# Kernel tuning notes

Hardware: AMD Instinct MI355X
Metric: run time of the kernel (lower is better)

Reference implementation:

```python
import jax, jax.numpy as jnp
import numpy as np

T, M, K, B, H, L, V = 64, 256, 6, 256, 256, 128, 780
E = T * M
PAD = E  # padding slot in hidden buffer = Lorentz origin

def _to_lorentz_np(s):
    t = np.sqrt(1.0 + (s * s).sum(-1, keepdims=True))
    return np.concatenate([t, s], -1).astype(np.float32)

def setup_inputs() -> dict:
    rng = np.random.default_rng(0)
    def make_nei():
        idx = np.full((T, M, K), PAD, np.int64)
        w = np.zeros((T, M, K), np.float32)
        for t in range(T):
            deg = rng.integers(0, K + 1, size=M)
            if t == 0:
                deg[:] = 0  # no messages exist yet
            mask = np.arange(K)[None, :] < deg[:, None]
            cand = rng.integers(0, max(1, t * M), size=(M, K))  # only already-computed slots
            idx[t] = np.where(mask, cand, PAD)
            w[t] = mask.astype(np.float32)
            w[t, deg == 0, 0] = 1.0  # zero-neighbor case -> use origin padding (as in torch code)
        return idx.astype(np.int32), w
    nei_h_idx, nei_h_w = make_nei()
    nei_o_idx, nei_o_w = make_nei()
    return dict(
        wid=jnp.asarray(rng.integers(0, V, size=(T, M)), jnp.int32),
        nei_h_idx=jnp.asarray(nei_h_idx), nei_h_w=jnp.asarray(nei_h_w),
        nei_o_idx=jnp.asarray(nei_o_idx), nei_o_w=jnp.asarray(nei_o_w),
        batch_idx=jnp.asarray(rng.integers(0, B, size=(T, M)), jnp.int32),
        direction=jnp.asarray(rng.integers(0, 2, size=(T, M)), jnp.int32),
        pred_target=jnp.asarray(rng.integers(0, V, size=(T, M)), jnp.int32),
        root_wid=jnp.asarray(rng.integers(0, V, size=(B,)), jnp.int32),
        root_o_idx=jnp.asarray(rng.integers(0, E, size=(B, K)), jnp.int32),
        root_o_w=jnp.ones((B, K), jnp.float32),
        x_tree_vecs=jnp.asarray(_to_lorentz_np(rng.standard_normal((B, L - 1)) * 0.5)),
        embedding=jnp.asarray(_to_lorentz_np(rng.standard_normal((V, H - 1)) * 0.5)),
        W0=jnp.asarray(rng.standard_normal((H, H)) * 0.02, dtype=jnp.float32),
        b0=jnp.zeros((H,), jnp.float32),
        s0=jnp.asarray(np.log(10.0), jnp.float32),
        W1=jnp.asarray(rng.standard_normal((H, 2 * H - 1)) * 0.02, dtype=jnp.float32),
        b1=jnp.zeros((H,), jnp.float32),
        s1=jnp.asarray(np.log(10.0), jnp.float32),
        wcls=jnp.asarray(_to_lorentz_np(rng.standard_normal((V, H + L - 2)) * 0.5)),
        wbias=jnp.zeros((V,), jnp.float32),
        ucls=jnp.asarray(_to_lorentz_np(rng.standard_normal((2, 2 * H + L - 3)) * 0.5)),
        ubias=jnp.zeros((2,), jnp.float32),
    )

def _llinear(x, W, b, scale):
    # LorentzLinear: affine map, then rescale space part so output stays on the hyperboloid
    x = x @ W.T + b
    xs = x[..., 1:]
    time = jax.nn.sigmoid(x[..., :1]) * jnp.exp(scale) + 1.1
    sq = (time * time - 1.0) / jnp.clip((xs * xs).sum(-1, keepdims=True), 1e-8)
    return jnp.concatenate([time, xs * jnp.sqrt(sq)], -1)

def _mid_point(x, w):
    # Lorentz centroid: weighted mean renormalized to the manifold. x: [...,K,d], w: [...,K]
    ave = jnp.einsum('...k,...kd->...d', w, x) / jnp.clip(w.sum(-1, keepdims=True), 1e-8)
    inner = (ave[..., 1:] ** 2).sum(-1, keepdims=True) - ave[..., :1] ** 2  # <ave,ave>_L
    return ave / jnp.sqrt(jnp.clip(-inner, 1e-8))

def _concat(x, y):
    # hyperbolic concat: keep space parts, recompute time (dim = d1+d2-1)
    time = jnp.sqrt(jnp.clip(x[..., :1] ** 2 + y[..., :1] ** 2 - 1.0, 1e-8))
    return jnp.concatenate([time, x[..., 1:], y[..., 1:]], -1)

def _centroid(x, cls_pts, bias):
    # LorentzCentroidDistance logits: 2 + 2*<x, c>_L + bias
    inner = x[..., 1:] @ cls_pts[:, 1:].T - x[..., :1] * cls_pts[None, :, 0]
    return 2.0 + 2.0 * inner + bias

def _ce(scores, tgt):
    lp = jax.nn.log_softmax(scores, -1)
    return -jnp.take_along_axis(lp, tgt[:, None], axis=-1)[:, 0]

def _forward_core(wid, nei_h_idx, nei_h_w, nei_o_idx, nei_o_w, batch_idx, direction,
                  pred_target, root_wid, root_o_idx, root_o_w, x_tree_vecs, embedding,
                  W0, b0, s0, W1, b1, s1, wcls, wbias, ucls, ubias):
    hbuf0 = jnp.zeros((E + 1, H), jnp.float32).at[:, 0].set(1.0)  # all origin; slot E is padding

    def step(carry, xs_t):
        hbuf, t = carry
        wid_t, idx_t, w_t = xs_t
        cur_x = embedding[wid_t]                      # [M,H]
        h_nei = hbuf[idx_t]                           # [M,K,H] gather of prior messages
        h1 = _llinear(h_nei, W0, b0, s0)              # A0
        h1m = _mid_point(h1, w_t)                     # [M,H]
        new_h = _llinear(_concat(cur_x, h1m), W1, b1, s1)  # A1
        hbuf = jax.lax.dynamic_update_slice(hbuf, new_h, (t * M, 0))
        return (hbuf, t + jnp.int32(1)), new_h

    (hbuf, _), new_h = jax.lax.scan(step, (hbuf0, jnp.int32(0)), (wid, nei_h_idx, nei_h_w))
    new_h = new_h.reshape(E, H)
    cur_x = embedding[wid.reshape(E)]
    cur_o = _mid_point(hbuf[nei_o_idx.reshape(E, K)], nei_o_w.reshape(E, K))
    ctx = x_tree_vecs[batch_idx.reshape(E)]

    # word prediction: roots (origin hidden) + forward-direction messages
    origin = jnp.zeros((B, H), jnp.float32).at[:, 0].set(1.0)
    root_scores = _centroid(_concat(origin, x_tree_vecs), wcls, wbias)   # [B,V]
    msg_scores = _centroid(_concat(new_h, ctx), wcls, wbias)             # [E,V]
    pmask = direction.reshape(E).astype(jnp.float32)
    pt = pred_target.reshape(E)
    pred_loss = (_ce(root_scores, root_wid).sum() + (pmask * _ce(msg_scores, pt)).sum()) / B
    pred_hit = ((jnp.argmax(root_scores, -1) == root_wid).astype(jnp.float32).sum()
                + (pmask * (jnp.argmax(msg_scores, -1) == pt).astype(jnp.float32)).sum())
    pred_acc = pred_hit / (B + pmask.sum())

    # stop prediction: every message + final per-tree root entry (target 0)
    stop_h = _concat(_concat(cur_x, cur_o), ctx)                         # [E, 2H+L-2]
    root_o = _mid_point(hbuf[root_o_idx], root_o_w)
    stop_root = _concat(_concat(embedding[root_wid], root_o), x_tree_vecs)
    stop_scores = _centroid(jnp.concatenate([stop_h, stop_root], 0), ucls, ubias)
    stop_tgt = jnp.concatenate([direction.reshape(E), jnp.zeros((B,), jnp.int32)], 0)
    stop_loss = _ce(stop_scores, stop_tgt).sum() / B
    stop_acc = (jnp.argmax(stop_scores, -1) == stop_tgt).astype(jnp.float32).mean()
    return pred_loss, stop_loss, pred_acc, stop_acc

def reference(wid, nei_h_idx, nei_h_w, nei_o_idx, nei_o_w, batch_idx, direction,
              pred_target, root_wid, root_o_idx, root_o_w, x_tree_vecs, embedding,
              W0, b0, s0, W1, b1, s1, wcls, wbias, ucls, ubias):
    return _forward_core(wid, nei_h_idx, nei_h_w, nei_o_idx, nei_o_w, batch_idx, direction,
                         pred_target, root_wid, root_o_idx, root_o_w, x_tree_vecs, embedding,
                         W0, b0, s0, W1, b1, s1, wcls, wbias, ucls, ubias)
```

## Files before the change

### kernel.cpp

```cpp
#include <hip/hip_runtime.h>
#include <math.h>

#define T_ 64
#define M_ 256
#define K_ 6
#define B_ 256
#define H_ 256
#define L_ 128
#define V_ 780
#define E_ (T_*M_)
#define ZD 383
#define UD 638
#define KP 384
#define VP 832
#define TAG_PAD 0x7fffffffu

typedef unsigned short ushort_t;
typedef __attribute__((ext_vector_type(8))) _Float16 half8v;
typedef __attribute__((ext_vector_type(4))) _Float16 half4v;
typedef __attribute__((ext_vector_type(2))) _Float16 half2v;
typedef __attribute__((ext_vector_type(4))) float f32x4v;
typedef unsigned long long u64;


__device__ __forceinline__ float blk_sum(float v, float* red) {
    int j = threadIdx.x;
    #pragma unroll
    for (int o = 32; o > 0; o >>= 1) v += __shfl_down(v, o, 64);
    __syncthreads();
    if ((j & 63) == 0) red[j >> 6] = v;
    __syncthreads();
    return red[0] + red[1] + red[2] + red[3];
}

__device__ __forceinline__ float wave_sum(float v) {
    #pragma unroll
    for (int o = 32; o > 0; o >>= 1) v += __shfl_xor(v, o, 64);
    return v;
}

__device__ __forceinline__ _Float16 f2h(float x) { return (_Float16)x; }

__device__ __forceinline__ u64 llc_load8(const u64* p) {
    return __hip_atomic_load(p, __ATOMIC_RELAXED, __HIP_MEMORY_SCOPE_AGENT);
}
__device__ __forceinline__ void llc_store8(u64* p, u64 v) {
    __hip_atomic_store(p, v, __ATOMIC_RELAXED, __HIP_MEMORY_SCOPE_AGENT);
}


#define PREP_R0 ((E_ + 1) * H_)
#define PREP_RT ((E_ + 1) * 128)
#define PREP_R1 65536
#define PREP_R2 65536
#define PREP_R3 (VP * KP)
#define PREP_R4 65536
#define PREP_TOTAL (PREP_R0 + PREP_RT + PREP_R1 + PREP_R2 + PREP_R3 + PREP_R4)

__global__ __launch_bounds__(256) void prep_k(const float* __restrict__ W0,
                                              const float* __restrict__ W1,
                                              const float* __restrict__ wcls,
                                              float* __restrict__ hbuf,
                                              u64* __restrict__ hbuf2,
                                              _Float16* __restrict__ W0P,
                                              _Float16* __restrict__ W1HP,
                                              _Float16* __restrict__ Wh,
                                              float* __restrict__ W1T) {
    int idx = blockIdx.x * 256 + threadIdx.x;
    if (idx < PREP_R0) {
        hbuf[idx] = (idx >= E_ * H_ && (idx & (H_ - 1)) == 0) ? 1.f : 0.f;
        return;
    }
    idx -= PREP_R0;
    if (idx < PREP_RT) {
        int row = idx >> 7, cp = idx & 127;
        u64 val = 0ull;
        if (row == E_) {
            unsigned int lo = (cp == 0) ? 0x3C00u : 0u;
            val = ((u64)TAG_PAD << 32) | lo;
        }
        hbuf2[idx] = val;
        return;
    }
    idx -= PREP_RT;
    if (idx < PREP_R1) {
        int e = idx & 7, l = (idx >> 3) & 63, ks = (idx >> 9) & 7, nt = idx >> 12;
        int jj = nt * 16 + (l & 15);
        int ii = ks * 32 + (l >> 4) * 8 + e;
        W0P[idx] = f2h(W0[(size_t)jj * H_ + ii]);
        return;
    }
    idx -= PREP_R1;
    if (idx < PREP_R2) {
        int e = idx & 7, l = (idx >> 3) & 63, ks = (idx >> 9) & 7, nt = idx >> 12;
        int jj = nt * 16 + (l & 15);
        int ii = ks * 32 + (l >> 4) * 8 + e;
        float v = (ii == 0) ? W1[(size_t)jj * (2 * H_ - 1)]
                            : W1[(size_t)jj * (2 * H_ - 1) + 255 + ii];
        W1HP[idx] = f2h(v);
        return;
    }
    idx -= PREP_R2;
    if (idx < PREP_R3) {
        int v = idx / KP, k = idx - v * KP;
        float val = (v < V_ && k < ZD) ? wcls[(size_t)v * ZD + k] : 0.f;
        Wh[idx] = f2h(val);
        return;
    }
    idx -= PREP_R3;
    if (idx < PREP_R4) {
        int i = idx >> 8, j = idx & 255;
        W1T[idx] = (i >= 1) ? W1[(size_t)j * (2 * H_ - 1) + i] : 0.f;
    }
}


__global__ __launch_bounds__(256) void basew_k(const float* __restrict__ emb,
                                               const float* __restrict__ W1T,
                                               const float* __restrict__ b1,
                                               float* __restrict__ basew) {
    int v = blockIdx.x, j = threadIdx.x;
    __shared__ float cxs[256];
    cxs[j] = emb[(size_t)v * H_ + j];
    __syncthreads();
    float acc = b1[j];
    #pragma unroll 8
    for (int i = 1; i < 256; i++) acc = fmaf(cxs[i], W1T[i * 256 + j], acc);
    basew[(size_t)v * H_ + j] = acc;
}


__global__ __launch_bounds__(256, 1) void scan_flow(float* __restrict__ hbuf,
        u64* __restrict__ hbuf2,
        const _Float16* __restrict__ W0P, const float* __restrict__ b0, const float* __restrict__ s0p,
        const _Float16* __restrict__ W1HP, const float* __restrict__ s1p,
        const float* __restrict__ emb, const int* __restrict__ wid,
        const int* __restrict__ nhi, const float* __restrict__ nhw,
        const float* __restrict__ basew) {
    int tid = threadIdx.x;
    int w = tid >> 6, l = tid & 63;
    int quad = l >> 4, col = l & 15;
    int m = blockIdx.x;
    int j0 = 4 * l;
    int cp = tid & 127;
    int rsel = tid >> 7;

    __shared__ __align__(16) _Float16 hn16[16][264];
    __shared__ __align__(16) _Float16 zzs[4][264];
    __shared__ __align__(16) float Ys[6][256];
    __shared__ __align__(16) float y2s[256];

    half8v w0f[4][8], w1f[4][8];
    #pragma unroll
    for (int q = 0; q < 4; q++) {
        int nt = 4 * w + q;
        #pragma unroll
        for (int ks = 0; ks < 8; ks++) {
            w0f[q][ks] = *(const half8v*)(W0P + ((size_t)(nt * 8 + ks) * 64 + l) * 8);
            w1f[q][ks] = *(const half8v*)(W1HP + ((size_t)(nt * 8 + ks) * 64 + l) * 8);
        }
    }

    float es0 = expf(s0p[0]);
    float es1 = expf(s1p[0]);
    float4 bj4 = *(const float4*)(b0 + j0);

    unsigned int tagx[3];
    const u64* pp[3];
    u64 pvv[3];
    #pragma unroll
    for (int p = 0; p < 3; p++) {
        int row = 2 * p + rsel;
        int id = nhi[(size_t)m * K_ + row];
        tagx[p] = (id < E_) ? (unsigned int)(id >> 8) + 1u : TAG_PAD;
        pp[p] = hbuf2 + ((size_t)id << 7) + cp;
        pvv[p] = llc_load8(pp[p]);
    }

    for (int t = 0; t < T_; t++) {
        int e = t * M_ + m;
        const float* wp = nhw + e * K_;

        float wk[K_];
        #pragma unroll
        for (int k = 0; k < K_; k++) wk[k] = wp[k];
        int wde = wid[e];
        float4 bw4 = *(const float4*)(basew + (size_t)wde * H_ + j0);
        float cx0 = emb[(size_t)wde * H_];

        for (;;) {
            bool ok = ((unsigned int)(pvv[0] >> 32) == tagx[0])
                   && ((unsigned int)(pvv[1] >> 32) == tagx[1])
                   && ((unsigned int)(pvv[2] >> 32) == tagx[2]);
            if (ok) break;
            __builtin_amdgcn_s_sleep(1);
            #pragma unroll
            for (int p = 0; p < 3; p++)
                if ((unsigned int)(pvv[p] >> 32) != tagx[p]) pvv[p] = llc_load8(pp[p]);
        }
        #pragma unroll
        for (int p = 0; p < 3; p++)
            *(unsigned int*)&hn16[2 * p + rsel][cp * 2] = (unsigned int)pvv[p];
        __syncthreads();

        if (t + 1 < T_) {
            #pragma unroll
            for (int p = 0; p < 3; p++) {
                int row = 2 * p + rsel;
                int id = nhi[(size_t)(e + M_) * K_ + row];
                tagx[p] = (id < E_) ? (unsigned int)(id >> 8) + 1u : TAG_PAD;
                pp[p] = hbuf2 + ((size_t)id << 7) + cp;
                pvv[p] = llc_load8(pp[p]);
            }
        }

        f32x4v acc[4];
        #pragma unroll
        for (int q = 0; q < 4; q++) acc[q] = (f32x4v){0.f, 0.f, 0.f, 0.f};
        #pragma unroll
        for (int ks = 0; ks < 8; ks++) {
            half8v afr = *(const half8v*)&hn16[col][ks * 32 + quad * 8];
            #pragma unroll
            for (int q = 0; q < 4; q++)
                acc[q] = __builtin_amdgcn_mfma_f32_16x16x32_f16(afr, w0f[q][ks], acc[q], 0, 0, 0);
        }
        #pragma unroll
        for (int q = 0; q < 4; q++) {
            int nt = 4 * w + q;
            #pragma unroll
            for (int rr = 0; rr < 4; rr++) {
                int row = quad * 4 + rr;
                if (row < 6) Ys[row][nt * 16 + col] = acc[q][rr];
            }
        }
        __syncthreads();

        float y[K_][4];
        #pragma unroll
        for (int k = 0; k < K_; k++) {
            float4 yv = *(const float4*)&Ys[k][j0];
            y[k][0] = yv.x + bj4.x; y[k][1] = yv.y + bj4.y;
            y[k][2] = yv.z + bj4.z; y[k][3] = yv.w + bj4.w;
        }
        float c[K_];
        #pragma unroll
        for (int k = 0; k < K_; k++) {
            float cc = y[k][0] * y[k][0] + y[k][1] * y[k][1]
                     + y[k][2] * y[k][2] + y[k][3] * y[k][3];
            if (l == 0) cc -= y[k][0] * y[k][0];
            c[k] = cc;
        }
        #pragma unroll
        for (int o = 32; o > 0; o >>= 1) {
            #pragma unroll
            for (int k = 0; k < K_; k++) c[k] += __shfl_xor(c[k], o, 64);
        }
        float y0b[K_];
        #pragma unroll
        for (int k = 0; k < K_; k++) y0b[k] = __shfl(y[k][0], 0, 64);

        float ave[4] = {0.f, 0.f, 0.f, 0.f};
        float wsum = 0.f;
        #pragma unroll
        for (int k = 0; k < K_; k++) {
            float tm = es0 / (1.f + expf(-y0b[k])) + 1.1f;
            float sc = sqrtf((tm * tm - 1.f) / fmaxf(c[k], 1e-8f));
            #pragma unroll
            for (int c2 = 0; c2 < 4; c2++) {
                float h1v = (l == 0 && c2 == 0) ? tm : y[k][c2] * sc;
                ave[c2] += wk[k] * h1v;
            }
            wsum += wk[k];
        }
        float inv = 1.f / fmaxf(wsum, 1e-8f);
        float innl = 0.f;
        #pragma unroll
        for (int c2 = 0; c2 < 4; c2++) { ave[c2] *= inv; innl += ave[c2] * ave[c2]; }
        if (l == 0) innl -= 2.f * ave[0] * ave[0];
        float inner = wave_sum(innl);
        float rsc = 1.f / sqrtf(fmaxf(-inner, 1e-8f));

        #pragma unroll
        for (int c2 = 0; c2 < 4; c2++) {
            int j = j0 + c2;
            float h1m = ave[c2] * rsc;
            if (j == 0) {
                zzs[w][0] = f2h(sqrtf(fmaxf(cx0 * cx0 + h1m * h1m - 1.f, 1e-8f)));
            } else {
                zzs[w][j] = f2h(h1m);
            }
        }

        f32x4v a2[4];
        #pragma unroll
        for (int q = 0; q < 4; q++) a2[q] = (f32x4v){0.f, 0.f, 0.f, 0.f};
        #pragma unroll
        for (int ks = 0; ks < 8; ks++) {
            half8v zfr = *(const half8v*)&zzs[w][ks * 32 + quad * 8];
            #pragma unroll
            for (int q = 0; q < 4; q++)
                a2[q] = __builtin_amdgcn_mfma_f32_16x16x32_f16(zfr, w1f[q][ks], a2[q], 0, 0, 0);
        }
        if (quad == 0) {
            #pragma unroll
            for (int q = 0; q < 4; q++) y2s[(4 * w + q) * 16 + col] = a2[q][0];
        }
        __syncthreads();

        if (w == 0) {
            float4 y2v = *(const float4*)&y2s[j0];
            float y2[4] = {y2v.x + bw4.x, y2v.y + bw4.y, y2v.z + bw4.z, y2v.w + bw4.w};
            float c2s = y2[0] * y2[0] + y2[1] * y2[1] + y2[2] * y2[2] + y2[3] * y2[3];
            if (l == 0) c2s -= y2[0] * y2[0];
            float ssq2 = wave_sum(c2s);
            float y20 = __shfl(y2[0], 0, 64);
            float tm2 = es1 / (1.f + expf(-y20)) + 1.1f;
            float sc2 = sqrtf((tm2 * tm2 - 1.f) / fmaxf(ssq2, 1e-8f));
            float hv0 = (l == 0) ? tm2 : y2[0] * sc2;
            float hv1 = y2[1] * sc2, hv2 = y2[2] * sc2, hv3 = y2[3] * sc2;

            unsigned int tag = (unsigned int)t + 1u;
            union { half2v h; unsigned int u; } c01, c23;
            c01.h.x = f2h(hv0); c01.h.y = f2h(hv1);
            c23.h.x = f2h(hv2); c23.h.y = f2h(hv3);
            u64* pb = hbuf2 + ((size_t)e << 7) + 2 * l;
            llc_store8(pb,     ((u64)tag << 32) | c01.u);
            llc_store8(pb + 1, ((u64)tag << 32) | c23.u);

            float4 out4 = {hv0, hv1, hv2, hv3};
            *(float4*)(hbuf + (size_t)e * H_ + j0) = out4;
        }
    }
}


__global__ __launch_bounds__(256) void zbuild2(const float* __restrict__ hbuf,
                                               const float* __restrict__ xtv,
                                               const int* __restrict__ bidx,
                                               _Float16* __restrict__ Zh) {
    int e = blockIdx.x, j = threadIdx.x;
    int bi = bidx[e];
    _Float16* zr = Zh + (size_t)e * KP;
    if (j == 0) {
        float nh0 = hbuf[(size_t)e * H_];
        float c0  = xtv[(size_t)bi * L_];
        float z0  = sqrtf(fmaxf(nh0 * nh0 + c0 * c0 - 1.f, 1e-8f));
        zr[0] = f2h(-z0);
    } else {
        zr[j] = f2h(hbuf[(size_t)e * H_ + j]);
    }
    if (j < 128) {
        int c = 256 + j;
        float v = (c <= 382) ? xtv[(size_t)bi * L_ + (c - 255)] : 0.f;
        zr[c] = f2h(v);
    }
}


__global__ __launch_bounds__(256) void gemm_ce(const _Float16* __restrict__ Zh,
                                               const _Float16* __restrict__ Wh,
                                               const float* __restrict__ wbias,
                                               const int* __restrict__ pt,
                                               const int* __restrict__ dir,
                                               float* __restrict__ part) {
    __shared__ __align__(16) _Float16 As[64][392];
    __shared__ __align__(16) _Float16 Bsf[64][392];
    __shared__ __align__(16) float SCs[64][68];
    __shared__ float rmax[64], rsum[64], rval[64];
    __shared__ int   rargi[64];

    int tid = threadIdx.x;
    int w = tid >> 6, l = tid & 63;
    int r16 = l & 15, quad = l >> 4;
    int q8 = quad * 8;
    int m0 = blockIdx.x * 64;

    #pragma unroll
    for (int i = 0; i < 12; i++) {
        int u = tid + i * 256;
        int row = u / 48, c8 = (u % 48) * 8;
        *(uint4*)&As[row][c8] = *(const uint4*)(Zh + (size_t)(m0 + row) * KP + c8);
    }
    if (tid < 64) {
        rmax[tid] = -1e30f; rsum[tid] = 0.f; rargi[tid] = 0; rval[tid] = 0.f;
    }
    __syncthreads();

    for (int nt = 0; nt < 13; nt++) {
        int n0 = nt * 64;
        #pragma unroll
        for (int i = 0; i < 12; i++) {
            int u = tid + i * 256;
            int row = u / 48, c8 = (u % 48) * 8;
            *(uint4*)&Bsf[row][c8] = *(const uint4*)(Wh + (size_t)(n0 + row) * KP + c8);
        }
        __syncthreads();

        f32x4v acc[4];
        #pragma unroll
        for (int mt = 0; mt < 4; mt++) acc[mt] = (f32x4v){0.f, 0.f, 0.f, 0.f};
        #pragma unroll
        for (int ks = 0; ks < 12; ks++) {
            half8v bfr = *(const half8v*)&Bsf[w * 16 + r16][ks * 32 + q8];
            #pragma unroll
            for (int mt = 0; mt < 4; mt++) {
                half8v afr = *(const half8v*)&As[mt * 16 + r16][ks * 32 + q8];
                acc[mt] = __builtin_amdgcn_mfma_f32_16x16x32_f16(afr, bfr, acc[mt], 0, 0, 0);
            }
        }
        int ncol = n0 + w * 16 + r16;
        float bias = (ncol < V_) ? wbias[ncol] : 0.f;
        #pragma unroll
        for (int mt = 0; mt < 4; mt++) {
            #pragma unroll
            for (int rr = 0; rr < 4; rr++)
                SCs[mt * 16 + quad * 4 + rr][w * 16 + r16] = 2.f + 2.f * acc[mt][rr] + bias;
        }
        __syncthreads();

        {
            int row = tid >> 2, prt = tid & 3;
            int tg = pt[m0 + row];
            float vals[16];
            float lm = -1e30f; int li = 0;
            #pragma unroll
            for (int c = 0; c < 16; c++) {
                int nc = n0 + prt * 16 + c;
                float x = (nc < V_) ? SCs[row][prt * 16 + c] : -1e30f;
                vals[c] = x;
                if (x > lm) { lm = x; li = nc; }
                if (nc == tg) rval[row] = x;
            }
            #pragma unroll
            for (int o = 1; o < 4; o <<= 1) {
                float om = __shfl_xor(lm, o, 64);
                int   oi = __shfl_xor(li, o, 64);
                if (om > lm || (om == lm && oi < li)) { lm = om; li = oi; }
            }
            float ls = 0.f;
            #pragma unroll
            for (int c = 0; c < 16; c++) {
                int nc = n0 + prt * 16 + c;
                if (nc < V_) ls += expf(vals[c] - lm);
            }
            #pragma unroll
            for (int o = 1; o < 4; o <<= 1) ls += __shfl_xor(ls, o, 64);
            if (prt == 0) {
                float om = rmax[row], os = rsum[row];
                float nm = fmaxf(om, lm);
                rsum[row] = os * expf(om - nm) + ls * expf(lm - nm);
                if (lm > om) rargi[row] = li;
                rmax[row] = nm;
            }
        }
        __syncthreads();
    }

    if (tid < 64) {
        int e = m0 + tid;
        int tg = pt[e];
        float pm = (float)dir[e];
        float lse = rmax[tid] + logf(rsum[tid]);
        float lloss = pm * (lse - rval[tid]);
        float lhit  = pm * ((rargi[tid] == tg) ? 1.f : 0.f);
        float lpm   = pm;
        lloss = wave_sum(lloss);
        lhit  = wave_sum(lhit);
        lpm   = wave_sum(lpm);
        if (tid == 0) {
            float* pr = part + (size_t)blockIdx.x * 8;
            pr[0] = lloss; pr[1] = lhit; pr[2] = lpm;
            pr[3] = 0.f; pr[4] = 0.f;
        }
    }
}


__global__ __launch_bounds__(256) void stoproot_k(const float* __restrict__ hbuf,
        const float* __restrict__ emb, const float* __restrict__ xtv,
        const int* __restrict__ wid, const int* __restrict__ noi, const float* __restrict__ now_w,
        const int* __restrict__ bidx, const int* __restrict__ dir,
        const int* __restrict__ rwid, const int* __restrict__ roi, const float* __restrict__ row_w,
        const float* __restrict__ wcls, const float* __restrict__ wbias,
        const float* __restrict__ ucls, const float* __restrict__ ubias,
        float* __restrict__ part) {
    __shared__ float red[256];
    __shared__ int   redi[256];
    __shared__ float shs[4];
    __shared__ float ctxs[L_];
    __shared__ float sc[V_];
    __shared__ float red2[4][2];

    if (blockIdx.x < 256) {
        int w = threadIdx.x >> 6, l = threadIdx.x & 63;
        int wg = blockIdx.x * 4 + w;

        float ua0[4], ub0[4], ua1[4], ub1[4], uc0[2], uc1[2];
        #pragma unroll
        for (int s = 0; s < 4; s++) {
            int j = s * 64 + l;
            ua0[s] = ucls[j];        ub0[s] = ucls[255 + j];
            ua1[s] = ucls[UD + j];   ub1[s] = ucls[UD + 255 + j];
        }
        #pragma unroll
        for (int s = 0; s < 2; s++) {
            int j = s * 64 + l;
            uc0[s] = ucls[510 + j];  uc1[s] = ucls[UD + 510 + j];
        }
        float u00 = ucls[0], u10 = ucls[UD];
        float ubs0 = ubias[0], ubs1 = ubias[1];

        float lloss = 0.f, lhit = 0.f;
        for (int i = 0; i < 16; i++) {
            int e = wg * 16 + i;
            const int*   ip = noi + e * K_;
            const float* wp = now_w + e * K_;
            float ave[4] = {0.f, 0.f, 0.f, 0.f};
            float wsum = 0.f;
            #pragma unroll
            for (int k = 0; k < K_; k++) {
                int id = ip[k]; float wt = wp[k];
                wsum += wt;
                const float* hr = hbuf + (size_t)id * H_;
                #pragma unroll
                for (int s = 0; s < 4; s++) ave[s] += wt * hr[s * 64 + l];
            }
            float inv = 1.f / fmaxf(wsum, 1e-8f);
            float innl = 0.f;
            #pragma unroll
            for (int s = 0; s < 4; s++) { ave[s] *= inv; innl += ave[s] * ave[s]; }
            if (l == 0) innl -= 2.f * ave[0] * ave[0];
            float inner = wave_sum(innl);
            float cs = 1.f / sqrtf(fmaxf(-inner, 1e-8f));

            int we = wid[e], bi = bidx[e];
            const float* er = emb + (size_t)we * H_;
            const float* cr = xtv + (size_t)bi * L_;

            float p0 = 0.f, p1 = 0.f;
            #pragma unroll
            for (int s = 0; s < 4; s++) {
                float cx = er[s * 64 + l];
                float co = ave[s] * cs;
                if (s == 0 && l == 0) {
                    float ctx0 = cr[0];
                    float t1sq = fmaxf(cx * cx + co * co - 1.f, 1e-8f);
                    float sh0 = sqrtf(fmaxf(t1sq + ctx0 * ctx0 - 1.f, 1e-8f));
                    p0 += -sh0 * u00; p1 += -sh0 * u10;
                } else {
                    p0 += cx * ua0[s] + co * ub0[s];
                    p1 += cx * ua1[s] + co * ub1[s];
                }
                if (s < 2) {
                    int j = s * 64 + l;
                    if (j >= 1) {
                        float ctx = cr[j];
                        p0 += ctx * uc0[s]; p1 += ctx * uc1[s];
                    }
                }
            }
            p0 = wave_sum(p0); p1 = wave_sum(p1);
            if (l == 0) {
                float sc0 = 2.f + 2.f * p0 + ubs0;
                float sc1 = 2.f + 2.f * p1 + ubs1;
                int tgt = dir[e];
                float mm = fmaxf(sc0, sc1);
                float lse = mm + logf(expf(sc0 - mm) + expf(sc1 - mm));
                lloss += lse - ((tgt == 0) ? sc0 : sc1);
                int am = (sc1 > sc0) ? 1 : 0;
                lhit += (am == tgt) ? 1.f : 0.f;
            }
        }
        if (l == 0) { red2[w][0] = lloss; red2[w][1] = lhit; }
        __syncthreads();
        if (threadIdx.x == 0) {
            float* pr = part + (size_t)(256 + blockIdx.x) * 8;
            pr[0] = 0.f; pr[1] = 0.f; pr[2] = 0.f;
            pr[3] = red2[0][0] + red2[1][0] + red2[2][0] + red2[3][0];
            pr[4] = red2[0][1] + red2[1][1] + red2[2][1] + red2[3][1];
        }
    } else {
        int b = blockIdx.x - 256, j = threadIdx.x;
        float* pr = part + (size_t)(512 + b) * 8;

        const int*   ip = roi + b * K_;
        const float* wp = row_w + b * K_;
        float ave = 0.f, wsum = 0.f;
        #pragma unroll
        for (int k = 0; k < K_; k++) {
            int id = ip[k]; float w = wp[k];
            ave += w * hbuf[(size_t)id * H_ + j];
            wsum += w;
        }
        ave /= fmaxf(wsum, 1e-8f);
        float inner = blk_sum((j == 0) ? -ave * ave : ave * ave, red);
        float ro = ave / sqrtf(fmaxf(-inner, 1e-8f));

        int   rw = rwid[b];
        float er = emb[(size_t)rw * H_ + j];
        float ctxj = (j < L_) ? xtv[(size_t)b * L_ + j] : 0.f;
        if (j == 0) { shs[0] = er; shs[1] = ro; shs[2] = ctxj; }
        if (j < L_) ctxs[j] = ctxj;
        __syncthreads();
        float t1sq = fmaxf(shs[0] * shs[0] + shs[1] * shs[1] - 1.f, 1e-8f);
        float sh0  = sqrtf(fmaxf(t1sq + shs[2] * shs[2] - 1.f, 1e-8f));

        float p0, p1;
        if (j >= 1) {
            p0 = er * ucls[j] + ro * ucls[255 + j];
            p1 = er * ucls[UD + j] + ro * ucls[UD + 255 + j];
            if (j < L_) { p0 += ctxj * ucls[510 + j]; p1 += ctxj * ucls[UD + 510 + j]; }
        } else {
            p0 = -sh0 * ucls[0];
            p1 = -sh0 * ucls[UD];
        }
        float s0 = 2.f + 2.f * blk_sum(p0, red) + ubias[0];
        float s1 = 2.f + 2.f * blk_sum(p1, red) + ubias[1];
        if (j == 0) {
            float mm = fmaxf(s0, s1);
            float lse = mm + logf(expf(s0 - mm) + expf(s1 - mm));
            int am = (s1 > s0) ? 1 : 0;
            pr[3] = lse - s0;
            pr[4] = (am == 0) ? 1.f : 0.f;
        }

        float c0 = shs[2];
        float z0 = sqrtf(fmaxf(c0 * c0, 1e-8f));
        __syncthreads();
        for (int v = j; v < V_; v += 256) {
            const float* wv = wcls + (size_t)v * ZD;
            float d = -z0 * wv[0];
            for (int i = 1; i < L_; i++) d += ctxs[i] * wv[255 + i];
            sc[v] = 2.f + 2.f * d + wbias[v];
        }
        __syncthreads();
        float mx = -1e30f; int mi = 0;
        for (int v = j; v < V_; v += 256) { float x = sc[v]; if (x > mx) { mx = x; mi = v; } }
        red[j] = mx; redi[j] = mi;
        __syncthreads();
        for (int o = 128; o > 0; o >>= 1) {
            if (j < o) {
                float xo = red[j + o]; int io = redi[j + o];
                if (xo > red[j] || (xo == red[j] && io < redi[j])) { red[j] = xo; redi[j] = io; }
            }
            __syncthreads();
        }
        float gm = red[0]; int ga = redi[0];
        __syncthreads();
        float se = 0.f;
        for (int v = j; v < V_; v += 256) se += expf(sc[v] - gm);
        red[j] = se;
        __syncthreads();
        for (int o = 128; o > 0; o >>= 1) { if (j < o) red[j] += red[j + o]; __syncthreads(); }
        if (j == 0) {
            float lse = gm + logf(red[0]);
            pr[0] = lse - sc[rw];
            pr[1] = (ga == rw) ? 1.f : 0.f;
            pr[2] = 0.f;
        }
    }
}


__global__ __launch_bounds__(256) void finalize2(const float* __restrict__ part,
                                                 float* __restrict__ out) {
    int j = threadIdx.x;
    __shared__ float red[256][5];
    #pragma unroll
    for (int c = 0; c < 5; c++)
        red[j][c] = part[(size_t)j * 8 + c] + part[(size_t)(j + 256) * 8 + c]
                  + part[(size_t)(j + 512) * 8 + c];
    __syncthreads();
    for (int o = 128; o > 0; o >>= 1) {
        if (j < o) {
            #pragma unroll
            for (int c = 0; c < 5; c++) red[j][c] += red[j + o][c];
        }
        __syncthreads();
    }
    if (j == 0) {
        out[0] = red[0][0] / (float)B_;
        out[1] = red[0][3] / (float)B_;
        out[2] = red[0][1] / ((float)B_ + red[0][2]);
        out[3] = red[0][4] / (float)(E_ + B_);
    }
}


extern "C" void kernel_launch(void* const* d_in, const int* in_sizes, int n_in,
                              void* d_out, int out_size, void* d_ws, size_t ws_size,
                              hipStream_t stream) {
    const int*   wid   = (const int*)d_in[0];
    const int*   nhi   = (const int*)d_in[1];
    const float* nhw   = (const float*)d_in[2];
    const int*   noi   = (const int*)d_in[3];
    const float* now_w = (const float*)d_in[4];
    const int*   bidx  = (const int*)d_in[5];
    const int*   dir   = (const int*)d_in[6];
    const int*   pt    = (const int*)d_in[7];
    const int*   rwid  = (const int*)d_in[8];
    const int*   roi   = (const int*)d_in[9];
    const float* row_w = (const float*)d_in[10];
    const float* xtv   = (const float*)d_in[11];
    const float* emb   = (const float*)d_in[12];
    const float* W0    = (const float*)d_in[13];
    const float* b0    = (const float*)d_in[14];
    const float* s0    = (const float*)d_in[15];
    const float* W1    = (const float*)d_in[16];
    const float* b1    = (const float*)d_in[17];
    const float* s1    = (const float*)d_in[18];
    const float* wcls  = (const float*)d_in[19];
    const float* wbias = (const float*)d_in[20];
    const float* ucls  = (const float*)d_in[21];
    const float* ubias = (const float*)d_in[22];

    float* ws    = (float*)d_ws;
    float* hbuf  = ws;
    u64*   hbuf2 = (u64*)(hbuf + (size_t)(E_ + 1) * H_);
    float* part  = (float*)(hbuf2 + (size_t)(E_ + 1) * 128);
    float* basew = part + 768 * 8;
    float* W1T   = basew + (size_t)V_ * H_;
    _Float16* W0P  = (_Float16*)(W1T + 65536);
    _Float16* W1HP = W0P + 65536;
    _Float16* Zh   = W1HP + 65536;
    _Float16* Wh   = Zh + (size_t)E_ * KP;
    float* out  = (float*)d_out;

    prep_k<<<(PREP_TOTAL + 255) / 256, 256, 0, stream>>>(W0, W1, wcls, hbuf, hbuf2,
                                                         W0P, W1HP, Wh, W1T);
    basew_k<<<V_, 256, 0, stream>>>(emb, W1T, b1, basew);

    scan_flow<<<M_, 256, 0, stream>>>(hbuf, hbuf2, W0P, b0, s0, W1HP, s1,
                                      emb, wid, nhi, nhw, basew);

    zbuild2<<<E_, 256, 0, stream>>>(hbuf, xtv, bidx, Zh);
    gemm_ce<<<256, 256, 0, stream>>>(Zh, Wh, wbias, pt, dir, part);
    stoproot_k<<<512, 256, 0, stream>>>(hbuf, emb, xtv, wid, noi, now_w, bidx, dir,
                                        rwid, roi, row_w, wcls, wbias, ucls, ubias, part);
    finalize2<<<1, 256, 0, stream>>>(part, out);
}
```

Before: 589.5 us.

## Fuse Z-build and prediction GEMM+CE into scan kernel tail with tag-polled handoff

Drops the zbuild2 and gemm_ce launches. After its scan loop, each scan_flow block polls tagged fp16 hidden rows for its 64-row tile, builds the fp16 Z tile in shared memory and runs the MFMA GEMM with online softmax cross-entropy. It also stops zero-initialising the full fp32 hidden buffer, writing only the padding row, and adds a per-row tagged h0 buffer. The aim is to cut launch overhead and the Zh round trip through global memory and to overlap the tail with the scan, at the cost of much more LDS per block and spin-waiting on other blocks' results.

```diff
diff --git a/kernel.cpp b/kernel.cpp
--- a/kernel.cpp
+++ b/kernel.cpp
@@ -49,26 +49,28 @@
 }
 
 
-#define PREP_R0 ((E_ + 1) * H_)
+#define PREP_R0 H_
 #define PREP_RT ((E_ + 1) * 128)
+#define PREP_RH3 E_
 #define PREP_R1 65536
 #define PREP_R2 65536
 #define PREP_R3 (VP * KP)
 #define PREP_R4 65536
-#define PREP_TOTAL (PREP_R0 + PREP_RT + PREP_R1 + PREP_R2 + PREP_R3 + PREP_R4)
+#define PREP_TOTAL (PREP_R0 + PREP_RT + PREP_RH3 + PREP_R1 + PREP_R2 + PREP_R3 + PREP_R4)
 
 __global__ __launch_bounds__(256) void prep_k(const float* __restrict__ W0,
                                               const float* __restrict__ W1,
                                               const float* __restrict__ wcls,
                                               float* __restrict__ hbuf,
                                               u64* __restrict__ hbuf2,
+                                              u64* __restrict__ hbuf3,
                                               _Float16* __restrict__ W0P,
                                               _Float16* __restrict__ W1HP,
                                               _Float16* __restrict__ Wh,
                                               float* __restrict__ W1T) {
     int idx = blockIdx.x * 256 + threadIdx.x;
     if (idx < PREP_R0) {
-        hbuf[idx] = (idx >= E_ * H_ && (idx & (H_ - 1)) == 0) ? 1.f : 0.f;
+        hbuf[(size_t)E_ * H_ + idx] = (idx == 0) ? 1.f : 0.f;
         return;
     }
     idx -= PREP_R0;
@@ -83,6 +85,11 @@
         return;
     }
     idx -= PREP_RT;
+    if (idx < PREP_RH3) {
+        hbuf3[idx] = 0ull;
+        return;
+    }
+    idx -= PREP_RH3;
     if (idx < PREP_R1) {
         int e = idx & 7, l = (idx >> 3) & 63, ks = (idx >> 9) & 7, nt = idx >> 12;
         int jj = nt * 16 + (l & 15);
@@ -131,12 +138,16 @@
 
 
 __global__ __launch_bounds__(256, 1) void scan_flow(float* __restrict__ hbuf,
-        u64* __restrict__ hbuf2,
+        u64* __restrict__ hbuf2, u64* __restrict__ hbuf3,
         const _Float16* __restrict__ W0P, const float* __restrict__ b0, const float* __restrict__ s0p,
         const _Float16* __restrict__ W1HP, const float* __restrict__ s1p,
         const float* __restrict__ emb, const int* __restrict__ wid,
         const int* __restrict__ nhi, const float* __restrict__ nhw,
-        const float* __restrict__ basew) {
+        const float* __restrict__ basew,
+        const _Float16* __restrict__ Wh, const float* __restrict__ wbias,
+        const int* __restrict__ pt, const int* __restrict__ dir,
+        const int* __restrict__ bidx, const float* __restrict__ xtv,
+        float* __restrict__ part) {
     int tid = threadIdx.x;
     int w = tid >> 6, l = tid & 63;
     int quad = l >> 4, col = l & 15;
@@ -149,6 +160,11 @@
     __shared__ __align__(16) _Float16 zzs[4][264];
     __shared__ __align__(16) float Ys[6][256];
     __shared__ __align__(16) float y2s[256];
+    __shared__ __align__(16) _Float16 As[64][392];
+    __shared__ __align__(16) _Float16 Bsf[64][392];
+    __shared__ __align__(16) float SCs[64][68];
+    __shared__ float rmax[64], rsum[64], rval[64];
+    __shared__ int   rargi[64];
 
     half8v w0f[4][8], w1f[4][8];
     #pragma unroll
@@ -327,150 +343,166 @@
             llc_store8(pb,     ((u64)tag << 32) | c01.u);
             llc_store8(pb + 1, ((u64)tag << 32) | c23.u);
 
+            if (l == 0) {
+                union { float f; unsigned int u; } h0b; h0b.f = tm2;
+                llc_store8(hbuf3 + e, ((u64)tag << 32) | h0b.u);
+            }
+
             float4 out4 = {hv0, hv1, hv2, hv3};
             *(float4*)(hbuf + (size_t)e * H_ + j0) = out4;
         }
     }
-}
-
-
-__global__ __launch_bounds__(256) void zbuild2(const float* __restrict__ hbuf,
-                                               const float* __restrict__ xtv,
-                                               const int* __restrict__ bidx,
-                                               _Float16* __restrict__ Zh) {
-    int e = blockIdx.x, j = threadIdx.x;
-    int bi = bidx[e];
-    _Float16* zr = Zh + (size_t)e * KP;
-    if (j == 0) {
-        float nh0 = hbuf[(size_t)e * H_];
-        float c0  = xtv[(size_t)bi * L_];
-        float z0  = sqrtf(fmaxf(nh0 * nh0 + c0 * c0 - 1.f, 1e-8f));
-        zr[0] = f2h(-z0);
-    } else {
-        zr[j] = f2h(hbuf[(size_t)e * H_ + j]);
-    }
-    if (j < 128) {
-        int c = 256 + j;
-        float v = (c <= 382) ? xtv[(size_t)bi * L_ + (c - 255)] : 0.f;
-        zr[c] = f2h(v);
-    }
-}
-
-
-__global__ __launch_bounds__(256) void gemm_ce(const _Float16* __restrict__ Zh,
-                                               const _Float16* __restrict__ Wh,
-                                               const float* __restrict__ wbias,
-                                               const int* __restrict__ pt,
-                                               const int* __restrict__ dir,
-                                               float* __restrict__ part) {
-    __shared__ __align__(16) _Float16 As[64][392];
-    __shared__ __align__(16) _Float16 Bsf[64][392];
-    __shared__ __align__(16) float SCs[64][68];
-    __shared__ float rmax[64], rsum[64], rval[64];
-    __shared__ int   rargi[64];
-
-    int tid = threadIdx.x;
-    int w = tid >> 6, l = tid & 63;
-    int r16 = l & 15, quad = l >> 4;
-    int q8 = quad * 8;
-    int m0 = blockIdx.x * 64;
-
-    #pragma unroll
-    for (int i = 0; i < 12; i++) {
-        int u = tid + i * 256;
-        int row = u / 48, c8 = (u % 48) * 8;
-        *(uint4*)&As[row][c8] = *(const uint4*)(Zh + (size_t)(m0 + row) * KP + c8);
-    }
-    if (tid < 64) {
-        rmax[tid] = -1e30f; rsum[tid] = 0.f; rargi[tid] = 0; rval[tid] = 0.f;
-    }
-    __syncthreads();
-
-    for (int nt = 0; nt < 13; nt++) {
-        int n0 = nt * 64;
-        #pragma unroll
-        for (int i = 0; i < 12; i++) {
-            int u = tid + i * 256;
-            int row = u / 48, c8 = (u % 48) * 8;
-            *(uint4*)&Bsf[row][c8] = *(const uint4*)(Wh + (size_t)(n0 + row) * KP + c8);
-        }
-        __syncthreads();
-
-        f32x4v acc[4];
-        #pragma unroll
-        for (int mt = 0; mt < 4; mt++) acc[mt] = (f32x4v){0.f, 0.f, 0.f, 0.f};
-        #pragma unroll
-        for (int ks = 0; ks < 12; ks++) {
-            half8v bfr = *(const half8v*)&Bsf[w * 16 + r16][ks * 32 + q8];
+
+    {
+        int m0 = m * 64;
+
+        u64 gpv[32];
+        #pragma unroll
+        for (int i = 0; i < 32; i++) {
+            int p = tid + i * 256;
+            int row = p >> 7, cpp = p & 127;
+            gpv[i] = llc_load8(hbuf2 + ((size_t)(m0 + row) << 7) + cpp);
+        }
+        for (;;) {
+            bool ok = true;
+            #pragma unroll
+            for (int i = 0; i < 32; i++) {
+                int row = (tid + i * 256) >> 7;
+                unsigned int tg = (unsigned int)((m0 + row) >> 8) + 1u;
+                if ((unsigned int)(gpv[i] >> 32) != tg) ok = false;
+            }
+            if (ok) break;
+            __builtin_amdgcn_s_sleep(1);
+            #pragma unroll
+            for (int i = 0; i < 32; i++) {
+                int p = tid + i * 256;
+                int row = p >> 7, cpp = p & 127;
+                unsigned int tg = (unsigned int)((m0 + row) >> 8) + 1u;
+                if ((unsigned int)(gpv[i] >> 32) != tg)
+                    gpv[i] = llc_load8(hbuf2 + ((size_t)(m0 + row) << 7) + cpp);
+            }
+        }
+        #pragma unroll
+        for (int i = 0; i < 32; i++) {
+            int p = tid + i * 256;
+            int row = p >> 7, cpp = p & 127;
+            *(unsigned int*)&As[row][2 * cpp] = (unsigned int)gpv[i];
+        }
+        #pragma unroll
+        for (int i = 0; i < 16; i++) {
+            int p = tid + i * 256;
+            int row = p >> 6, k2 = (p & 63) * 2;
+            int bi = bidx[m0 + row];
+            int ca = 256 + k2;
+            half2v hv;
+            hv.x = (ca <= 382) ? f2h(xtv[(size_t)bi * L_ + (ca - 255)]) : (_Float16)0.f;
+            hv.y = (ca + 1 <= 382) ? f2h(xtv[(size_t)bi * L_ + (ca - 254)]) : (_Float16)0.f;
+            *(half2v*)&As[row][ca] = hv;
+        }
+        if (tid < 64) {
+            int e2 = m0 + tid;
+            unsigned int tg = (unsigned int)(e2 >> 8) + 1u;
+            u64 hv3 = llc_load8(hbuf3 + e2);
+            while ((unsigned int)(hv3 >> 32) != tg) {
+                __builtin_amdgcn_s_sleep(1);
+                hv3 = llc_load8(hbuf3 + e2);
+            }
+            union { unsigned int u; float f; } h0c; h0c.u = (unsigned int)hv3;
+            int bi = bidx[e2];
+            float c0 = xtv[(size_t)bi * L_];
+            float z0 = sqrtf(fmaxf(h0c.f * h0c.f + c0 * c0 - 1.f, 1e-8f));
+            As[tid][0] = f2h(-z0);
+            rmax[tid] = -1e30f; rsum[tid] = 0.f; rargi[tid] = 0; rval[tid] = 0.f;
+        }
+        __syncthreads();
+
+        int q8 = quad * 8;
+        for (int nt = 0; nt < 13; nt++) {
+            int n0 = nt * 64;
+            #pragma unroll
+            for (int i = 0; i < 12; i++) {
+                int uu = tid + i * 256;
+                int row = uu / 48, c8 = (uu % 48) * 8;
+                *(uint4*)&Bsf[row][c8] = *(const uint4*)(Wh + (size_t)(n0 + row) * KP + c8);
+            }
+            __syncthreads();
+
+            f32x4v gacc[4];
+            #pragma unroll
+            for (int mt = 0; mt < 4; mt++) gacc[mt] = (f32x4v){0.f, 0.f, 0.f, 0.f};
+            #pragma unroll
+            for (int ks = 0; ks < 12; ks++) {
+                half8v bfr = *(const half8v*)&Bsf[w * 16 + col][ks * 32 + q8];
+                #pragma unroll
+                for (int mt = 0; mt < 4; mt++) {
+                    half8v afr = *(const half8v*)&As[mt * 16 + col][ks * 32 + q8];
+                    gacc[mt] = __builtin_amdgcn_mfma_f32_16x16x32_f16(afr, bfr, gacc[mt], 0, 0, 0);
+                }
+            }
+            int ncol = n0 + w * 16 + col;
+            float bias = (ncol < V_) ? wbias[ncol] : 0.f;
             #pragma unroll
             for (int mt = 0; mt < 4; mt++) {
-                half8v afr = *(const half8v*)&As[mt * 16 + r16][ks * 32 + q8];
-                acc[mt] = __builtin_amdgcn_mfma_f32_16x16x32_f16(afr, bfr, acc[mt], 0, 0, 0);
-            }
-        }
-        int ncol = n0 + w * 16 + r16;
-        float bias = (ncol < V_) ? wbias[ncol] : 0.f;
-        #pragma unroll
-        for (int mt = 0; mt < 4; mt++) {
-            #pragma unroll
-            for (int rr = 0; rr < 4; rr++)
-                SCs[mt * 16 + quad * 4 + rr][w * 16 + r16] = 2.f + 2.f * acc[mt][rr] + bias;
-        }
-        __syncthreads();
-
-        {
-            int row = tid >> 2, prt = tid & 3;
-            int tg = pt[m0 + row];
-            float vals[16];
-            float lm = -1e30f; int li = 0;
-            #pragma unroll
-            for (int c = 0; c < 16; c++) {
-                int nc = n0 + prt * 16 + c;
-                float x = (nc < V_) ? SCs[row][prt * 16 + c] : -1e30f;
-                vals[c] = x;
-                if (x > lm) { lm = x; li = nc; }
-                if (nc == tg) rval[row] = x;
-            }
-            #pragma unroll
-            for (int o = 1; o < 4; o <<= 1) {
-                float om = __shfl_xor(lm, o, 64);
-                int   oi = __shfl_xor(li, o, 64);
-                if (om > lm || (om == lm && oi < li)) { lm = om; li = oi; }
-            }
-            float ls = 0.f;
-            #pragma unroll
-            for (int c = 0; c < 16; c++) {
-                int nc = n0 + prt * 16 + c;
-                if (nc < V_) ls += expf(vals[c] - lm);
-            }
-            #pragma unroll
-            for (int o = 1; o < 4; o <<= 1) ls += __shfl_xor(ls, o, 64);
-            if (prt == 0) {
-                float om = rmax[row], os = rsum[row];
-                float nm = fmaxf(om, lm);
-                rsum[row] = os * expf(om - nm) + ls * expf(lm - nm);
-                if (lm > om) rargi[row] = li;
-                rmax[row] = nm;
-            }
-        }
-        __syncthreads();
-    }
-
-    if (tid < 64) {
-        int e = m0 + tid;
-        int tg = pt[e];
-        float pm = (float)dir[e];
-        float lse = rmax[tid] + logf(rsum[tid]);
-        float lloss = pm * (lse - rval[tid]);
-        float lhit  = pm * ((rargi[tid] == tg) ? 1.f : 0.f);
-        float lpm   = pm;
-        lloss = wave_sum(lloss);
-        lhit  = wave_sum(lhit);
-        lpm   = wave_sum(lpm);
-        if (tid == 0) {
-            float* pr = part + (size_t)blockIdx.x * 8;
-            pr[0] = lloss; pr[1] = lhit; pr[2] = lpm;
-            pr[3] = 0.f; pr[4] = 0.f;
+                #pragma unroll
+                for (int rr = 0; rr < 4; rr++)
+                    SCs[mt * 16 + quad * 4 + rr][w * 16 + col] = 2.f + 2.f * gacc[mt][rr] + bias;
+            }
+            __syncthreads();
+
+            {
+                int row = tid >> 2, prt = tid & 3;
+                int tg = pt[m0 + row];
+                float vals[16];
+                float lm = -1e30f; int li = 0;
+                #pragma unroll
+                for (int cc = 0; cc < 16; cc++) {
+                    int nc = n0 + prt * 16 + cc;
+                    float x = (nc < V_) ? SCs[row][prt * 16 + cc] : -1e30f;
+                    vals[cc] = x;
+                    if (x > lm) { lm = x; li = nc; }
+                    if (nc == tg) rval[row] = x;
+                }
+                #pragma unroll
+                for (int o = 1; o < 4; o <<= 1) {
+                    float om = __shfl_xor(lm, o, 64);
+                    int   oi = __shfl_xor(li, o, 64);
+                    if (om > lm || (om == lm && oi < li)) { lm = om; li = oi; }
+                }
+                float ls = 0.f;
+                #pragma unroll
+                for (int cc = 0; cc < 16; cc++) {
+                    int nc = n0 + prt * 16 + cc;
+                    if (nc < V_) ls += expf(vals[cc] - lm);
+                }
+                #pragma unroll
+                for (int o = 1; o < 4; o <<= 1) ls += __shfl_xor(ls, o, 64);
+                if (prt == 0) {
+                    float om = rmax[row], os = rsum[row];
+                    float nm = fmaxf(om, lm);
+                    rsum[row] = os * expf(om - nm) + ls * expf(lm - nm);
+                    if (lm > om) rargi[row] = li;
+                    rmax[row] = nm;
+                }
+            }
+            __syncthreads();
+        }
+
+        if (tid < 64) {
+            int e2 = m0 + tid;
+            int tg = pt[e2];
+            float pm = (float)dir[e2];
+            float lse = rmax[tid] + logf(rsum[tid]);
+            float lloss = pm * (lse - rval[tid]);
+            float lhit  = pm * ((rargi[tid] == tg) ? 1.f : 0.f);
+            float lpm   = pm;
+            lloss = wave_sum(lloss);
+            lhit  = wave_sum(lhit);
+            lpm   = wave_sum(lpm);
+            if (tid == 0) {
+                float* pr = part + (size_t)m * 8;
+                pr[0] = lloss; pr[1] = lhit; pr[2] = lpm;
+                pr[3] = 0.f; pr[4] = 0.f;
+            }
         }
     }
 }
@@ -717,24 +749,23 @@
     float* ws    = (float*)d_ws;
     float* hbuf  = ws;
     u64*   hbuf2 = (u64*)(hbuf + (size_t)(E_ + 1) * H_);
-    float* part  = (float*)(hbuf2 + (size_t)(E_ + 1) * 128);
+    u64*   hbuf3 = hbuf2 + (size_t)(E_ + 1) * 128;
+    float* part  = (float*)(hbuf3 + E_);
     float* basew = part + 768 * 8;
     float* W1T   = basew + (size_t)V_ * H_;
     _Float16* W0P  = (_Float16*)(W1T + 65536);
     _Float16* W1HP = W0P + 65536;
-    _Float16* Zh   = W1HP + 65536;
-    _Float16* Wh   = Zh + (size_t)E_ * KP;
+    _Float16* Wh   = W1HP + 65536;
     float* out  = (float*)d_out;
 
-    prep_k<<<(PREP_TOTAL + 255) / 256, 256, 0, stream>>>(W0, W1, wcls, hbuf, hbuf2,
+    prep_k<<<(PREP_TOTAL + 255) / 256, 256, 0, stream>>>(W0, W1, wcls, hbuf, hbuf2, hbuf3,
                                                          W0P, W1HP, Wh, W1T);
     basew_k<<<V_, 256, 0, stream>>>(emb, W1T, b1, basew);
 
-    scan_flow<<<M_, 256, 0, stream>>>(hbuf, hbuf2, W0P, b0, s0, W1HP, s1,
-                                      emb, wid, nhi, nhw, basew);
-
-    zbuild2<<<E_, 256, 0, stream>>>(hbuf, xtv, bidx, Zh);
-    gemm_ce<<<256, 256, 0, stream>>>(Zh, Wh, wbias, pt, dir, part);
+    scan_flow<<<M_, 256, 0, stream>>>(hbuf, hbuf2, hbuf3, W0P, b0, s0, W1HP, s1,
+                                      emb, wid, nhi, nhw, basew,
+                                      Wh, wbias, pt, dir, bidx, xtv, part);
+
     stoproot_k<<<512, 256, 0, stream>>>(hbuf, emb, xtv, wid, noi, now_w, bidx, dir,
                                         rwid, roi, row_w, wcls, wbias, ucls, ubias, part);
     finalize2<<<1, 256, 0, stream>>>(part, out);
```

New measurement: 575.4 us. -2.4%, faster.
